# Optimization experiments

Measured on AMD Instinct MI355X. Metric: run time of the kernel, lower is better.

Reference implementation:

```python
import jax, jax.numpy as jnp
import numpy as np

BS, IN_F, OUT_F = 1024, 128, 100000
M, S, ALPHA = 0.35, 30.0, 0.5


def _l2norm(x):
    # F.normalize: x / max(||x||, eps)
    n = jnp.sqrt(jnp.sum(x * x, axis=-1, keepdims=True))
    return x / jnp.maximum(n, 1e-12)


def setup_inputs() -> dict:
    key = jax.random.key(0)
    k1, k2, k3 = jax.random.split(key, 3)
    return {
        "input": jax.random.normal(k1, (BS, IN_F), dtype=jnp.float32),
        "label": jax.random.randint(k2, (BS,), 0, OUT_F, dtype=jnp.int64),
        "weight": jax.random.normal(k3, (OUT_F, IN_F), dtype=jnp.float32),
    }


def reference(input, label, weight):
    wn = _l2norm(weight)                      # [nc, d]
    fn = _l2norm(input)                       # [bs, d]
    logits = jnp.einsum('bd,cd->bc', fn, wn)  # [bs, nc] cosine sims
    bs = fn.shape[0]
    rows = jnp.arange(bs)

    pos = jnp.take_along_axis(logits, label[:, None], axis=1)[:, 0] * S  # [bs]
    # negatives: all classes except the label (replaces masked_select + view)
    neg = (logits * S).at[rows, label].set(-jnp.inf)
    lse_neg = jax.nn.logsumexp(neg, axis=1)   # [bs]

    # loss = mean(log(1 + exp(m + lse_neg - pos)))
    loss = jnp.mean(jax.nn.softplus(M + lse_neg - pos))

    # weight.data update: per-class mean of normalized features for classes
    # present in the batch (the torch loop is exactly a segment-mean; note
    # weight_update aliases weight.data so the final blend is a no-op and the
    # result is simply: present rows <- class mean, other rows unchanged).
    sums = jax.ops.segment_sum(fn, label, num_segments=OUT_F)                # [nc, d]
    counts = jax.ops.segment_sum(jnp.ones((bs,), fn.dtype), label, num_segments=OUT_F)
    present = counts > 0
    class_mean = sums / jnp.maximum(counts, 1.0)[:, None]
    new_weight = jnp.where(present[:, None], class_mean, weight)

    return loss, new_weight
```

## Files before the change

kernel.cpp:

```cpp
#include <hip/hip_runtime.h>

#define BS 1024
#define D 128
#define NC 100000
#define NCP 100096
#define NTILES 782
#define S_SCALE 30.0f
#define MARGIN 0.35f
#define GRIDX 64

typedef __attribute__((ext_vector_type(8))) short bf16x8;
typedef __attribute__((ext_vector_type(4))) float f32x4;

__device__ __forceinline__ unsigned short f2bf(float f) {
    union { float f; unsigned u; } x; x.f = f;
    unsigned u = x.u;
    u += 0x7FFFu + ((u >> 16) & 1u);
    return (unsigned short)(u >> 16);
}

__device__ __forceinline__ void gld_lds16(const void* g, void* l) {
    auto gp = (const __attribute__((address_space(1))) unsigned int*)(g);
    auto lp = (__attribute__((address_space(3))) unsigned int*)(l);
    __builtin_amdgcn_global_load_lds(gp, lp, 16, 0, 0);
}

__global__ void prep_fn(const float* __restrict__ inp, const int* __restrict__ label,
                        const float* __restrict__ wt,
                        float* __restrict__ fn_f32, unsigned short* __restrict__ fn_sw,
                        float* __restrict__ counts, float* __restrict__ pos) {
    int row = blockIdx.x;
    int lane = threadIdx.x;
    float2 v = *(const float2*)(inp + row * D + lane * 2);
    float s = v.x * v.x + v.y * v.y;
    #pragma unroll
    for (int m = 1; m < 64; m <<= 1) s += __shfl_xor(s, m);
    float inv = 1.0f / fmaxf(sqrtf(s), 1e-12f);
    float a = v.x * inv, b = v.y * inv;
    *(float2*)(fn_f32 + row * D + lane * 2) = make_float2(a, b);
    unsigned pack = (unsigned)f2bf(a) | ((unsigned)f2bf(b) << 16);
    ((unsigned*)fn_sw)[row * 64 + (((lane >> 2) ^ (row & 15)) << 2) + (lane & 3)] = pack;

    int c = label[row];
    float2 wv = *(const float2*)(wt + c * D + lane * 2);
    float sw_ = wv.x * wv.x + wv.y * wv.y;
    float dt  = wv.x * a + wv.y * b;
    #pragma unroll
    for (int m = 1; m < 64; m <<= 1) { sw_ += __shfl_xor(sw_, m); dt += __shfl_xor(dt, m); }
    if (lane == 0) {
        float invw = 1.0f / fmaxf(sqrtf(sw_), 1e-12f);
        pos[row] = S_SCALE * dt * invw;
        atomicAdd(counts + c, 1.0f);
    }
}

__global__ void prep_wn(const float* __restrict__ wt, const float* __restrict__ counts,
                        unsigned short* __restrict__ wn_sw, float* __restrict__ outw) {
    int wv = threadIdx.x >> 6, lane = threadIdx.x & 63;
    int row = blockIdx.x * 4 + wv;
    int t = row >> 7, c = row & 127;
    unsigned* dst = (unsigned*)wn_sw + t * 8192 + c * 64 +
                    (((lane >> 2) ^ (c & 15)) << 2) + (lane & 3);
    if (row < NC) {
        float2 v = *(const float2*)(wt + row * D + lane * 2);
        float s = v.x * v.x + v.y * v.y;
        #pragma unroll
        for (int m = 1; m < 64; m <<= 1) s += __shfl_xor(s, m);
        float inv = 1.0f / fmaxf(sqrtf(s), 1e-12f);
        *dst = (unsigned)f2bf(v.x * inv) | ((unsigned)f2bf(v.y * inv) << 16);
        float cnt = counts[row];
        float2 o = (cnt > 0.0f) ? make_float2(0.0f, 0.0f) : v;
        *(float2*)(outw + row * D + lane * 2) = o;
    } else {
        *dst = 0u;
    }
}

__global__ __launch_bounds__(256, 2) void main_gemm(
    const unsigned short* __restrict__ fnsw, const unsigned short* __restrict__ wnsw,
    float* __restrict__ sumexp) {
    __shared__ __align__(16) short As[128 * 128];
    __shared__ __align__(16) short Bs[128 * 128];
    int tid = threadIdx.x;
    int lane = tid & 63, w = tid >> 6;
    int quad = lane >> 4, l15 = lane & 15;
    int m0 = (w >> 1) * 64, n0 = (w & 1) * 64;
    int rowbase = blockIdx.y * 128;

    {
        const char* gA = (const char*)fnsw + rowbase * 256 + w * 8192 + lane * 16;
        char* lA = (char*)As + w * 8192;
        #pragma unroll
        for (int j = 0; j < 8; j++) gld_lds16(gA + j * 1024, lA + j * 1024);
    }

    float sums[16];
    #pragma unroll
    for (int i = 0; i < 16; i++) sums[i] = 0.0f;

    for (int tile = blockIdx.x; tile < NTILES; tile += GRIDX) {
        const char* gB = (const char*)wnsw + tile * 32768 + w * 8192 + lane * 16;
        char* lB = (char*)Bs + w * 8192;
        __syncthreads();
        #pragma unroll
        for (int j = 0; j < 8; j++) gld_lds16(gB + j * 1024, lB + j * 1024);
        __syncthreads();

        f32x4 acc[4][4];
        #pragma unroll
        for (int mt = 0; mt < 4; mt++)
            #pragma unroll
            for (int nt = 0; nt < 4; nt++)
                acc[mt][nt] = (f32x4){0.0f, 0.0f, 0.0f, 0.0f};

        #pragma unroll
        for (int ks = 0; ks < 4; ks++) {
            int kb = ks * 4 + quad;
            bf16x8 af[4], bf[4];
            #pragma unroll
            for (int mt = 0; mt < 4; mt++) {
                int row = m0 + mt * 16 + l15;
                af[mt] = *(const bf16x8*)(As + (row * 16 + (kb ^ l15)) * 8);
            }
            #pragma unroll
            for (int nt = 0; nt < 4; nt++) {
                int row = n0 + nt * 16 + l15;
                bf[nt] = *(const bf16x8*)(Bs + (row * 16 + (kb ^ l15)) * 8);
            }
            #pragma unroll
            for (int mt = 0; mt < 4; mt++)
                #pragma unroll
                for (int nt = 0; nt < 4; nt++)
                    acc[mt][nt] = __builtin_amdgcn_mfma_f32_16x16x32_bf16(
                        af[mt], bf[nt], acc[mt][nt], 0, 0, 0);
        }

        #pragma unroll
        for (int nt = 0; nt < 4; nt++)
            #pragma unroll
            for (int mt = 0; mt < 4; mt++)
                #pragma unroll
                for (int r = 0; r < 4; r++)
                    sums[mt * 4 + r] += __expf(fmaf(acc[mt][nt][r], S_SCALE, -30.0f));
    }

    #pragma unroll
    for (int mt = 0; mt < 4; mt++) {
        #pragma unroll
        for (int r = 0; r < 4; r++) {
            float s = sums[mt * 4 + r];
            s += __shfl_xor(s, 1);
            s += __shfl_xor(s, 2);
            s += __shfl_xor(s, 4);
            s += __shfl_xor(s, 8);
            if (l15 == 0)
                atomicAdd(sumexp + rowbase + m0 + mt * 16 + quad * 4 + r, s);
        }
    }
}

__global__ void loss_k(const float* __restrict__ sumexp, const float* __restrict__ pos,
                       float* __restrict__ out) {
    __shared__ float red[256];
    int t = threadIdx.x;
    float acc = 0.0f;
    #pragma unroll
    for (int i = 0; i < 4; i++) {
        int r = t + i * 256;
        float p = pos[r];
        float sneg = fmaxf(sumexp[r] - __expf(p - 30.0f), 1e-38f);
        float lse = 30.0f + logf(sneg);
        float z = MARGIN + lse - p;
        acc += fmaxf(z, 0.0f) + log1pf(__expf(-fabsf(z)));
    }
    red[t] = acc;
    __syncthreads();
    for (int s = 128; s > 0; s >>= 1) {
        if (t < s) red[t] += red[t + s];
        __syncthreads();
    }
    if (t == 0) out[0] = red[0] * (1.0f / 1024.0f);
}

__global__ void addmean_k(const float* __restrict__ fn_f32, const int* __restrict__ label,
                          const float* __restrict__ counts, float* __restrict__ outw) {
    int b = blockIdx.x, t = threadIdx.x;
    int c = label[b];
    float cnt = counts[c];
    atomicAdd(outw + c * D + t, fn_f32[b * D + t] / cnt);
}

extern "C" void kernel_launch(void* const* d_in, const int* in_sizes, int n_in,
                              void* d_out, int out_size, void* d_ws, size_t ws_size,
                              hipStream_t stream) {
    (void)in_sizes; (void)n_in; (void)out_size; (void)ws_size;
    const float* inp   = (const float*)d_in[0];
    const int*   label = (const int*)d_in[1];
    const float* wt    = (const float*)d_in[2];
    float* out = (float*)d_out;

    char* w = (char*)d_ws;
    float*          fn_f32 = (float*)(w);
    unsigned short* fn_sw  = (unsigned short*)(w + 524288);
    unsigned short* wn_sw  = (unsigned short*)(w + 786432);
    float*          sumexp = (float*)(w + 26411008);
    float*          counts = (float*)(w + 26415104);
    float*          pos    = (float*)(w + 26815104);

    hipMemsetAsync(w + 26411008, 0, 404096, stream);

    prep_fn<<<BS, 64, 0, stream>>>(inp, label, wt, fn_f32, fn_sw, counts, pos);
    prep_wn<<<NCP / 4, 256, 0, stream>>>(wt, counts, wn_sw, out + 1);
    main_gemm<<<dim3(GRIDX, 8), 256, 0, stream>>>(fn_sw, wn_sw, sumexp);
    addmean_k<<<BS, D, 0, stream>>>(fn_f32, label, counts, out + 1);
    loss_k<<<1, 256, 0, stream>>>(sumexp, pos, out);
}
```

Baseline: 163.7 us.

## Double-buffer B tiles, keep A fragments in registers, use native exp2

The main GEMM now keeps the A (feature) fragments for all k-steps in registers, so the A shared-memory buffer can be reused as a second B buffer. B tiles are double-buffered, with the next tile's global-to-LDS load issued before computing on the current one, and only one barrier per iteration. The exp is computed with a raw exp2 builtin using a prescaled constant, which drops one multiply per element. The register-resident A fragments raise register pressure under the launch bound of two blocks, which risks spills or lower occupancy.

```diff
diff --git a/kernel.cpp b/kernel.cpp
--- a/kernel.cpp
+++ b/kernel.cpp
@@ -8,6 +8,7 @@
 #define S_SCALE 30.0f
 #define MARGIN 0.35f
 #define GRIDX 64
+#define S2LOG2E 43.2808512f
 
 typedef __attribute__((ext_vector_type(8))) short bf16x8;
 typedef __attribute__((ext_vector_type(4))) float f32x4;
@@ -79,8 +80,7 @@
 __global__ __launch_bounds__(256, 2) void main_gemm(
     const unsigned short* __restrict__ fnsw, const unsigned short* __restrict__ wnsw,
     float* __restrict__ sumexp) {
-    __shared__ __align__(16) short As[128 * 128];
-    __shared__ __align__(16) short Bs[128 * 128];
+    __shared__ __align__(16) short Bs[2][128 * 128];
     int tid = threadIdx.x;
     int lane = tid & 63, w = tid >> 6;
     int quad = lane >> 4, l15 = lane & 15;
@@ -89,22 +89,45 @@
 
     {
         const char* gA = (const char*)fnsw + rowbase * 256 + w * 8192 + lane * 16;
-        char* lA = (char*)As + w * 8192;
+        char* lA = (char*)Bs[0] + w * 8192;
         #pragma unroll
         for (int j = 0; j < 8; j++) gld_lds16(gA + j * 1024, lA + j * 1024);
     }
+    __syncthreads();
+
+    bf16x8 af[4][4];
+    #pragma unroll
+    for (int ks = 0; ks < 4; ks++) {
+        int kb = ks * 4 + quad;
+        #pragma unroll
+        for (int mt = 0; mt < 4; mt++) {
+            int row = m0 + mt * 16 + l15;
+            af[ks][mt] = *(const bf16x8*)(&Bs[0][0] + (row * 16 + (kb ^ l15)) * 8);
+        }
+    }
+    __syncthreads();
 
     float sums[16];
     #pragma unroll
     for (int i = 0; i < 16; i++) sums[i] = 0.0f;
 
+    {
+        const char* gB = (const char*)wnsw + blockIdx.x * 32768 + w * 8192 + lane * 16;
+        char* lB = (char*)Bs[0] + w * 8192;
+        #pragma unroll
+        for (int j = 0; j < 8; j++) gld_lds16(gB + j * 1024, lB + j * 1024);
+    }
+    __syncthreads();
+
+    int cur = 0;
     for (int tile = blockIdx.x; tile < NTILES; tile += GRIDX) {
-        const char* gB = (const char*)wnsw + tile * 32768 + w * 8192 + lane * 16;
-        char* lB = (char*)Bs + w * 8192;
-        __syncthreads();
-        #pragma unroll
-        for (int j = 0; j < 8; j++) gld_lds16(gB + j * 1024, lB + j * 1024);
-        __syncthreads();
+        int nxt = tile + GRIDX;
+        if (nxt < NTILES) {
+            const char* gB = (const char*)wnsw + nxt * 32768 + w * 8192 + lane * 16;
+            char* lB = (char*)Bs[cur ^ 1] + w * 8192;
+            #pragma unroll
+            for (int j = 0; j < 8; j++) gld_lds16(gB + j * 1024, lB + j * 1024);
+        }
 
         f32x4 acc[4][4];
         #pragma unroll
@@ -113,26 +136,22 @@
             for (int nt = 0; nt < 4; nt++)
                 acc[mt][nt] = (f32x4){0.0f, 0.0f, 0.0f, 0.0f};
 
+        const short* B = &Bs[cur][0];
         #pragma unroll
         for (int ks = 0; ks < 4; ks++) {
             int kb = ks * 4 + quad;
-            bf16x8 af[4], bf[4];
-            #pragma unroll
-            for (int mt = 0; mt < 4; mt++) {
-                int row = m0 + mt * 16 + l15;
-                af[mt] = *(const bf16x8*)(As + (row * 16 + (kb ^ l15)) * 8);
-            }
+            bf16x8 bf[4];
             #pragma unroll
             for (int nt = 0; nt < 4; nt++) {
                 int row = n0 + nt * 16 + l15;
-                bf[nt] = *(const bf16x8*)(Bs + (row * 16 + (kb ^ l15)) * 8);
+                bf[nt] = *(const bf16x8*)(B + (row * 16 + (kb ^ l15)) * 8);
             }
             #pragma unroll
             for (int mt = 0; mt < 4; mt++)
                 #pragma unroll
                 for (int nt = 0; nt < 4; nt++)
                     acc[mt][nt] = __builtin_amdgcn_mfma_f32_16x16x32_bf16(
-                        af[mt], bf[nt], acc[mt][nt], 0, 0, 0);
+                        af[ks][mt], bf[nt], acc[mt][nt], 0, 0, 0);
         }
 
         #pragma unroll
@@ -141,7 +160,11 @@
             for (int mt = 0; mt < 4; mt++)
                 #pragma unroll
                 for (int r = 0; r < 4; r++)
-                    sums[mt * 4 + r] += __expf(fmaf(acc[mt][nt][r], S_SCALE, -30.0f));
+                    sums[mt * 4 + r] +=
+                        __builtin_amdgcn_exp2f(fmaf(acc[mt][nt][r], S2LOG2E, -S2LOG2E));
+
+        __syncthreads();
+        cur ^= 1;
     }
 
     #pragma unroll
```

After: 167.3 us. 1.02x slower.

## Load MFMA fragments directly from global memory in fragment-native layout, drop LDS staging

Applied to the files above, without the earlier changes.

Repacks the normalized features and weights into an MFMA fragment-ordered layout so each wave loads its A and B operands straight from global memory into registers, removing LDS staging and block barriers. The A tile for 64 rows stays in registers for the whole loop, and B fragments for the next tile are prefetched while the current MFMAs run. The grid becomes 48x16, exp is replaced with a raw exp2 using a folded scale, and per-wave row sums are combined in shared memory before one atomic per row. In exchange there is more register pressure at 3 blocks per CU, and each B tile is now reread from global/L2 by 16 row-blocks instead of 8.

```diff
diff --git a/kernel.cpp b/kernel.cpp
--- a/kernel.cpp
+++ b/kernel.cpp
@@ -7,7 +7,9 @@
 #define NTILES 782
 #define S_SCALE 30.0f
 #define MARGIN 0.35f
-#define GRIDX 64
+#define GRIDX 48
+#define GRIDY 16
+#define S2LOG2E 43.2808512f
 
 typedef __attribute__((ext_vector_type(8))) short bf16x8;
 typedef __attribute__((ext_vector_type(4))) float f32x4;
@@ -19,15 +21,10 @@
     return (unsigned short)(u >> 16);
 }
 
-__device__ __forceinline__ void gld_lds16(const void* g, void* l) {
-    auto gp = (const __attribute__((address_space(1))) unsigned int*)(g);
-    auto lp = (__attribute__((address_space(3))) unsigned int*)(l);
-    __builtin_amdgcn_global_load_lds(gp, lp, 16, 0, 0);
-}
 
 __global__ void prep_fn(const float* __restrict__ inp, const int* __restrict__ label,
                         const float* __restrict__ wt,
-                        float* __restrict__ fn_f32, unsigned short* __restrict__ fn_sw,
+                        float* __restrict__ fn_f32, unsigned short* __restrict__ fn_fr,
                         float* __restrict__ counts, float* __restrict__ pos) {
     int row = blockIdx.x;
     int lane = threadIdx.x;
@@ -39,7 +36,7 @@
     float a = v.x * inv, b = v.y * inv;
     *(float2*)(fn_f32 + row * D + lane * 2) = make_float2(a, b);
     unsigned pack = (unsigned)f2bf(a) | ((unsigned)f2bf(b) << 16);
-    ((unsigned*)fn_sw)[row * 64 + (((lane >> 2) ^ (row & 15)) << 2) + (lane & 3)] = pack;
+    ((unsigned*)fn_fr)[(row >> 4) * 1024 + (lane >> 2) * 64 + ((row & 15) << 2) + (lane & 3)] = pack;
 
     int c = label[row];
     float2 wv = *(const float2*)(wt + c * D + lane * 2);
@@ -55,12 +52,11 @@
 }
 
 __global__ void prep_wn(const float* __restrict__ wt, const float* __restrict__ counts,
-                        unsigned short* __restrict__ wn_sw, float* __restrict__ outw) {
+                        unsigned short* __restrict__ wn_fr, float* __restrict__ outw) {
     int wv = threadIdx.x >> 6, lane = threadIdx.x & 63;
     int row = blockIdx.x * 4 + wv;
-    int t = row >> 7, c = row & 127;
-    unsigned* dst = (unsigned*)wn_sw + t * 8192 + c * 64 +
-                    (((lane >> 2) ^ (c & 15)) << 2) + (lane & 3);
+    unsigned* dst = (unsigned*)wn_fr + (row >> 4) * 1024 + (lane >> 2) * 64 +
+                    ((row & 15) << 2) + (lane & 3);
     if (row < NC) {
         float2 v = *(const float2*)(wt + row * D + lane * 2);
         float s = v.x * v.x + v.y * v.y;
@@ -76,72 +72,73 @@
     }
 }
 
-__global__ __launch_bounds__(256, 2) void main_gemm(
-    const unsigned short* __restrict__ fnsw, const unsigned short* __restrict__ wnsw,
+__global__ __launch_bounds__(256, 3) void main_gemm(
+    const unsigned short* __restrict__ fnfr, const unsigned short* __restrict__ wnfr,
     float* __restrict__ sumexp) {
-    __shared__ __align__(16) short As[128 * 128];
-    __shared__ __align__(16) short Bs[128 * 128];
+    __shared__ float red[256];
     int tid = threadIdx.x;
     int lane = tid & 63, w = tid >> 6;
     int quad = lane >> 4, l15 = lane & 15;
-    int m0 = (w >> 1) * 64, n0 = (w & 1) * 64;
-    int rowbase = blockIdx.y * 128;
-
+    int rowbase = blockIdx.y * 64;
+
+    bf16x8 af[4][4];
     {
-        const char* gA = (const char*)fnsw + rowbase * 256 + w * 8192 + lane * 16;
-        char* lA = (char*)As + w * 8192;
-        #pragma unroll
-        for (int j = 0; j < 8; j++) gld_lds16(gA + j * 1024, lA + j * 1024);
+        const char* gA = (const char*)fnfr + (rowbase >> 4) * 4096 + lane * 16;
+        #pragma unroll
+        for (int mt = 0; mt < 4; mt++)
+            #pragma unroll
+            for (int ks = 0; ks < 4; ks++)
+                af[ks][mt] = *(const bf16x8*)(gA + mt * 4096 + ks * 1024);
     }
 
     float sums[16];
     #pragma unroll
     for (int i = 0; i < 16; i++) sums[i] = 0.0f;
 
+    const char* gB = (const char*)wnfr + (size_t)blockIdx.x * 32768 + w * 8192 + lane * 16;
+    const long long step = (long long)GRIDX * 32768;
+
+    bf16x8 b[2][4];
+    #pragma unroll
+    for (int nt = 0; nt < 2; nt++)
+        #pragma unroll
+        for (int ks = 0; ks < 4; ks++)
+            b[nt][ks] = *(const bf16x8*)(gB + nt * 4096 + ks * 1024);
+
     for (int tile = blockIdx.x; tile < NTILES; tile += GRIDX) {
-        const char* gB = (const char*)wnsw + tile * 32768 + w * 8192 + lane * 16;
-        char* lB = (char*)Bs + w * 8192;
-        __syncthreads();
-        #pragma unroll
-        for (int j = 0; j < 8; j++) gld_lds16(gB + j * 1024, lB + j * 1024);
-        __syncthreads();
-
-        f32x4 acc[4][4];
+        f32x4 acc[4][2];
         #pragma unroll
         for (int mt = 0; mt < 4; mt++)
             #pragma unroll
-            for (int nt = 0; nt < 4; nt++)
+            for (int nt = 0; nt < 2; nt++)
                 acc[mt][nt] = (f32x4){0.0f, 0.0f, 0.0f, 0.0f};
 
         #pragma unroll
-        for (int ks = 0; ks < 4; ks++) {
-            int kb = ks * 4 + quad;
-            bf16x8 af[4], bf[4];
-            #pragma unroll
-            for (int mt = 0; mt < 4; mt++) {
-                int row = m0 + mt * 16 + l15;
-                af[mt] = *(const bf16x8*)(As + (row * 16 + (kb ^ l15)) * 8);
-            }
-            #pragma unroll
-            for (int nt = 0; nt < 4; nt++) {
-                int row = n0 + nt * 16 + l15;
-                bf[nt] = *(const bf16x8*)(Bs + (row * 16 + (kb ^ l15)) * 8);
-            }
+        for (int ks = 0; ks < 4; ks++)
             #pragma unroll
             for (int mt = 0; mt < 4; mt++)
                 #pragma unroll
-                for (int nt = 0; nt < 4; nt++)
+                for (int nt = 0; nt < 2; nt++)
                     acc[mt][nt] = __builtin_amdgcn_mfma_f32_16x16x32_bf16(
-                        af[mt], bf[nt], acc[mt][nt], 0, 0, 0);
+                        af[ks][mt], b[nt][ks], acc[mt][nt], 0, 0, 0);
+
+        gB += step;
+        if (tile + GRIDX < NTILES) {
+            #pragma unroll
+            for (int nt = 0; nt < 2; nt++)
+                #pragma unroll
+                for (int ks = 0; ks < 4; ks++)
+                    b[nt][ks] = *(const bf16x8*)(gB + nt * 4096 + ks * 1024);
         }
 
         #pragma unroll
-        for (int nt = 0; nt < 4; nt++)
-            #pragma unroll
-            for (int mt = 0; mt < 4; mt++)
+        for (int mt = 0; mt < 4; mt++)
+            #pragma unroll
+            for (int nt = 0; nt < 2; nt++)
                 #pragma unroll
                 for (int r = 0; r < 4; r++)
-                    sums[mt * 4 + r] += __expf(fmaf(acc[mt][nt][r], S_SCALE, -30.0f));
+                    sums[mt * 4 + r] +=
+                        __builtin_amdgcn_exp2f(fmaf(acc[mt][nt][r], S2LOG2E, -S2LOG2E));
     }
 
     #pragma unroll
@@ -153,9 +150,13 @@
             s += __shfl_xor(s, 2);
             s += __shfl_xor(s, 4);
             s += __shfl_xor(s, 8);
-            if (l15 == 0)
-                atomicAdd(sumexp + rowbase + m0 + mt * 16 + quad * 4 + r, s);
+            if (l15 == 0) red[w * 64 + mt * 16 + quad * 4 + r] = s;
         }
+    }
+    __syncthreads();
+    if (tid < 64) {
+        float s = red[tid] + red[64 + tid] + red[128 + tid] + red[192 + tid];
+        atomicAdd(sumexp + rowbase + tid, s);
     }
 }
 
@@ -201,17 +202,17 @@
 
     char* w = (char*)d_ws;
     float*          fn_f32 = (float*)(w);
-    unsigned short* fn_sw  = (unsigned short*)(w + 524288);
-    unsigned short* wn_sw  = (unsigned short*)(w + 786432);
+    unsigned short* fn_fr  = (unsigned short*)(w + 524288);
+    unsigned short* wn_fr  = (unsigned short*)(w + 786432);
     float*          sumexp = (float*)(w + 26411008);
     float*          counts = (float*)(w + 26415104);
     float*          pos    = (float*)(w + 26815104);
 
     hipMemsetAsync(w + 26411008, 0, 404096, stream);
 
-    prep_fn<<<BS, 64, 0, stream>>>(inp, label, wt, fn_f32, fn_sw, counts, pos);
-    prep_wn<<<NCP / 4, 256, 0, stream>>>(wt, counts, wn_sw, out + 1);
-    main_gemm<<<dim3(GRIDX, 8), 256, 0, stream>>>(fn_sw, wn_sw, sumexp);
+    prep_fn<<<BS, 64, 0, stream>>>(inp, label, wt, fn_f32, fn_fr, counts, pos);
+    prep_wn<<<NCP / 4, 256, 0, stream>>>(wt, counts, wn_fr, out + 1);
+    main_gemm<<<dim3(GRIDX, GRIDY), 256, 0, stream>>>(fn_fr, wn_fr, sumexp);
     addmean_k<<<BS, D, 0, stream>>>(fn_f32, label, counts, out + 1);
     loss_k<<<1, 256, 0, stream>>>(sumexp, pos, out);
 }
```

Result: faster. 157.5 us (-3.8%).
